# Optimization experiments

Measured on AMD Instinct MI355X. Metric: run time of the kernel, lower is better.

The kernel has to match this reference:

```python
import jax, jax.numpy as jnp
import numpy as np


def _gcn(x, edge_index, W, b):
    # PyG GCNConv, improved=True: A_hat = A + 2I, sym norm D^-1/2 A_hat D^-1/2
    N = x.shape[0]
    src, dst = edge_index[0], edge_index[1]
    h = x @ W  # [N, F]
    deg = jax.ops.segment_sum(jnp.ones(src.shape[0], x.dtype), dst, num_segments=N) + 2.0
    dinv = jax.lax.rsqrt(deg)
    norm = dinv[src] * dinv[dst]  # per-edge coefficient (edge_weight = 1)
    agg = jax.ops.segment_sum(h[src] * norm[:, None], dst, num_segments=N)
    agg = agg + (2.0 * dinv * dinv)[:, None] * h  # self loops, weight 2
    return agg + b


def _gclstm(x, H, C, Wx, Th, bch, wc, b):
    # GCLSTM with K=1: ChebConv on H reduces to H @ Theta + cheb_bias.
    # Gate order in stacked params: [i, f, c, o]; wc order: [i, f, o].
    gx = (jnp.einsum('nf,gfh->gnh', x, Wx)
          + jnp.einsum('nf,gfh->gnh', H, Th)
          + bch[:, None, :] + b[:, None, :])  # [4, N, F]
    I = jax.nn.sigmoid(gx[0] + wc[0] * C)
    Fg = jax.nn.sigmoid(gx[1] + wc[1] * C)
    Cn = Fg * C + I * jnp.tanh(gx[2])
    O = jax.nn.sigmoid(gx[3] + wc[2] * Cn)
    Hn = O * jnp.tanh(Cn)
    return Hn, Cn


def setup_inputs() -> dict:
    key = jax.random.key(0)
    ks = jax.random.split(key, 16)
    F = 2048
    E = 131072
    s = 0.02  # keep gates away from saturation
    inp = {
        'x': jax.random.normal(ks[0], (F, F), jnp.float32),
        'edge_index': jax.random.randint(ks[1], (2, E), 0, F),
        'no_pedestrians': F,
        'gcn1_w': s * jax.random.normal(ks[2], (F, F), jnp.float32),
        'gcn1_b': s * jax.random.normal(ks[3], (F,), jnp.float32),
        'gcn2_w': s * jax.random.normal(ks[4], (F, F), jnp.float32),
        'gcn2_b': s * jax.random.normal(ks[5], (F,), jnp.float32),
        'lstm_Wx': s * jax.random.normal(ks[6], (3, 4, F, F), jnp.float32),
        'lstm_Th': s * jax.random.normal(ks[7], (3, 4, F, F), jnp.float32),
        'lstm_bch': s * jax.random.normal(ks[8], (3, 4, F), jnp.float32),
        'lstm_wc': s * jax.random.normal(ks[9], (3, 3, F), jnp.float32),
        'lstm_b': s * jax.random.normal(ks[10], (3, 4, F), jnp.float32),
        'lin_w': s * jax.random.normal(ks[11], (9, F), jnp.float32),
        'lin_b': s * jax.random.normal(ks[12], (9,), jnp.float32),
    }
    return inp


def reference(x, edge_index, no_pedestrians, gcn1_w, gcn1_b, gcn2_w, gcn2_b,
              lstm_Wx, lstm_Th, lstm_bch, lstm_wc, lstm_b, lin_w, lin_b):
    # x is already [input_feat, input_feat], so the zero-padding in the
    # original forward is a no-op.
    h = jax.nn.relu(_gcn(x, edge_index, gcn1_w, gcn1_b))
    h = jax.nn.relu(_gcn(h, edge_index, gcn2_w, gcn2_b))
    N, F = h.shape
    z = jnp.zeros((N, F), h.dtype)
    H = h
    for l in range(3):  # 3 structurally distinct GCLSTM layers, single step
        H, _C = _gclstm(H, z, z, lstm_Wx[l], lstm_Th[l], lstm_bch[l], lstm_wc[l], lstm_b[l])
    h = jax.nn.relu(H)
    y = h @ lin_w.T + lin_b  # [N, 9]
    P = int(no_pedestrians)
    out = jax.nn.log_softmax(y[:P].reshape(P, 3, 3), axis=-1)  # LogSoftmax(dim=1) on each [3,3]
    return out
```

## Files before the change

### kernel.cpp

```cpp
#include <hip/hip_runtime.h>
#include <stdint.h>


#define FDIM 2048
typedef unsigned short u16;
typedef unsigned int u32;

typedef __bf16 bf16x8 __attribute__((ext_vector_type(8)));
typedef float f32x4 __attribute__((ext_vector_type(4)));
typedef __attribute__((address_space(1))) void* as1p;
typedef __attribute__((address_space(3))) void* as3p;

__device__ __forceinline__ float bflo(u32 u) { return __uint_as_float(u << 16); }
__device__ __forceinline__ float bfhi(u32 u) { return __uint_as_float(u & 0xffff0000u); }
__device__ __forceinline__ u16 f2b(float f) {
    u32 u = __float_as_uint(f);
    return (u16)((u + 0x7fffu + ((u >> 16) & 1u)) >> 16);
}
__device__ __forceinline__ void unp8(const uint4 v, float* f) {
    f[0] = bflo(v.x); f[1] = bfhi(v.x); f[2] = bflo(v.y); f[3] = bfhi(v.y);
    f[4] = bflo(v.z); f[5] = bfhi(v.z); f[6] = bflo(v.w); f[7] = bfhi(v.w);
}
__device__ __forceinline__ uint4 pk8(const float* f) {
    uint4 v;
    v.x = (u32)f2b(f[0]) | ((u32)f2b(f[1]) << 16);
    v.y = (u32)f2b(f[2]) | ((u32)f2b(f[3]) << 16);
    v.z = (u32)f2b(f[4]) | ((u32)f2b(f[5]) << 16);
    v.w = (u32)f2b(f[6]) | ((u32)f2b(f[7]) << 16);
    return v;
}

__global__ void k_zero(int* __restrict__ p, int n) {
    int i = blockIdx.x * 256 + threadIdx.x;
    if (i < n) p[i] = 0;
}

__global__ void k_hist(const int* __restrict__ ei, int* __restrict__ counts, int ne) {
    int e = blockIdx.x * 256 + threadIdx.x;
    if (e < ne) atomicAdd(&counts[ei[ne + e]], 1);
}

__global__ __launch_bounds__(1024) void k_scan(const int* __restrict__ counts,
                                               int* __restrict__ off,
                                               float* __restrict__ dinv) {
    __shared__ int sb[2][FDIM];
    const int t = threadIdx.x;
    const int c0 = counts[t], c1 = counts[t + 1024];
    sb[0][t] = c0; sb[0][t + 1024] = c1;
    __syncthreads();
    int cur = 0;
    for (int st = 1; st < FDIM; st <<= 1) {
        const int i1 = t + 1024;
        int v0 = sb[cur][t] + (t >= st ? sb[cur][t - st] : 0);
        int v1 = sb[cur][i1] + (i1 >= st ? sb[cur][i1 - st] : 0);
        sb[cur ^ 1][t] = v0; sb[cur ^ 1][i1] = v1;
        __syncthreads();
        cur ^= 1;
    }
    off[t] = sb[cur][t] - c0;
    off[t + 1024] = sb[cur][t + 1024] - c1;
    if (t == 0) off[FDIM] = sb[cur][FDIM - 1];
    dinv[t] = rsqrtf((float)c0 + 2.0f);
    dinv[t + 1024] = rsqrtf((float)c1 + 2.0f);
}

__global__ void k_fill(const int* __restrict__ ei, const int* __restrict__ off,
                       int* __restrict__ cursor, const float* __restrict__ dinv,
                       int* __restrict__ csr_s, float* __restrict__ csr_w, int ne) {
    int e = blockIdx.x * 256 + threadIdx.x;
    if (e >= ne) return;
    int s = ei[e], d = ei[ne + e];
    int p = atomicAdd(&cursor[d], 1);
    int idx = off[d] + p;
    csr_s[idx] = s;
    csr_w[idx] = dinv[s] * dinv[d];
}

__global__ void k_f2b8(const float* __restrict__ x, u16* __restrict__ o) {
    const int i = blockIdx.x * 256 + threadIdx.x;
    const size_t base = (size_t)i * 8;
    float f[8];
    *(float4*)(f)     = *(const float4*)(x + base);
    *(float4*)(f + 4) = *(const float4*)(x + base + 4);
    *(uint4*)(o + base) = pk8(f);
}

__global__ __launch_bounds__(1024) void k_transp(const float* __restrict__ W,
                                                 u16* __restrict__ Wt) {
    __shared__ float tile[32][33];
    const int tx = threadIdx.x & 31, ty = threadIdx.x >> 5;
    const int bx = blockIdx.x * 32, by = blockIdx.y * 32;
    tile[ty][tx] = W[(size_t)(by + ty) * FDIM + bx + tx];
    __syncthreads();
    Wt[(size_t)(bx + ty) * FDIM + by + tx] = f2b(tile[tx][ty]);
}

struct GemmArgs {
    const u16* A;
    const u16* Bt[3];
    u16* C[3];
    const float* b1[3];
    const float* b2[3];
};

__global__ __launch_bounds__(256) void k_gemm(GemmArgs ga) {
    const int z = blockIdx.z;
    const u16* __restrict__ A  = ga.A;
    const u16* __restrict__ Bt = ga.Bt[z];

    const int tid = threadIdx.x;
    const int wid = tid >> 6;
    const int lane = tid & 63;
    const int wr = wid >> 1, wc = wid & 1;
    const int lr = lane & 15, lg = lane >> 4;
    const int brow = blockIdx.y * 128;
    const int bcol = blockIdx.x * 128;

    __shared__ u16 As[128 * 32];
    __shared__ u16 Bs[128 * 32];

    f32x4 acc[4][4];
#pragma unroll
    for (int m = 0; m < 4; ++m)
#pragma unroll
        for (int n = 0; n < 4; ++n) acc[m][n] = (f32x4){0.f, 0.f, 0.f, 0.f};

    const u16* gA[2]; const u16* gB[2];
    u16* lA[2]; u16* lB[2];
#pragma unroll
    for (int q = 0; q < 2; ++q) {
        const int seg = q * 4 + wid;
        const int row = seg * 16 + (lane >> 2);
        const int ke  = (lane & 3) * 8;
        gA[q] = A  + (size_t)(brow + row) * FDIM + ke;
        gB[q] = Bt + (size_t)(bcol + row) * FDIM + ke;
        lA[q] = As + seg * 512;
        lB[q] = Bs + seg * 512;
    }

    int aoff[4], boff[4];
#pragma unroll
    for (int m = 0; m < 4; ++m) aoff[m] = (wr * 64 + m * 16 + lr) * 32 + lg * 8;
#pragma unroll
    for (int n = 0; n < 4; ++n) boff[n] = (wc * 64 + n * 16 + lr) * 32 + lg * 8;

    for (int kt = 0; kt < FDIM / 32; ++kt) {
        const int ko = kt * 32;
        __builtin_amdgcn_global_load_lds((as1p)(u16*)(gA[0] + ko), (as3p)lA[0], 16, 0, 0);
        __builtin_amdgcn_global_load_lds((as1p)(u16*)(gA[1] + ko), (as3p)lA[1], 16, 0, 0);
        __builtin_amdgcn_global_load_lds((as1p)(u16*)(gB[0] + ko), (as3p)lB[0], 16, 0, 0);
        __builtin_amdgcn_global_load_lds((as1p)(u16*)(gB[1] + ko), (as3p)lB[1], 16, 0, 0);
        __syncthreads();

        bf16x8 av[4], bv[4];
#pragma unroll
        for (int m = 0; m < 4; ++m) av[m] = *reinterpret_cast<const bf16x8*>(&As[aoff[m]]);
#pragma unroll
        for (int n = 0; n < 4; ++n) bv[n] = *reinterpret_cast<const bf16x8*>(&Bs[boff[n]]);
#pragma unroll
        for (int m = 0; m < 4; ++m)
#pragma unroll
            for (int n = 0; n < 4; ++n)
                acc[m][n] = __builtin_amdgcn_mfma_f32_16x16x32_bf16(av[m], bv[n], acc[m][n], 0, 0, 0);
        __syncthreads();
    }

    u16* __restrict__ C = ga.C[z];
    const float* b1 = ga.b1[z];
    const float* b2 = ga.b2[z];
#pragma unroll
    for (int n = 0; n < 4; ++n) {
        const int col = bcol + wc * 64 + n * 16 + lr;
        float badd = 0.f;
        if (b1) badd = b1[col] + b2[col];
#pragma unroll
        for (int m = 0; m < 4; ++m) {
            const int row0 = brow + wr * 64 + m * 16 + lg * 4;
#pragma unroll
            for (int r = 0; r < 4; ++r)
                C[(size_t)(row0 + r) * FDIM + col] = f2b(acc[m][n][r] + badd);
        }
    }
}

__global__ __launch_bounds__(256) void k_gather(
    const u16* __restrict__ Hp, const int* __restrict__ off,
    const int* __restrict__ csr_s, const float* __restrict__ csr_w,
    const float* __restrict__ dinv, const float* __restrict__ bias,
    u16* __restrict__ outb) {
    const int n = blockIdx.x, t = threadIdx.x;
    __shared__ int s_src[256];
    __shared__ float s_w[256];
    float acc[8] = {0.f, 0.f, 0.f, 0.f, 0.f, 0.f, 0.f, 0.f};
    const int e0 = off[n], e1 = off[n + 1];
    const int fb = t * 8;
    for (int base = e0; base < e1; base += 256) {
        const int cnt = min(256, e1 - base);
        __syncthreads();
        if (t < cnt) { s_src[t] = csr_s[base + t]; s_w[t] = csr_w[base + t]; }
        __syncthreads();
        for (int i = 0; i < cnt; ++i) {
            const int s = s_src[i];
            const float w = s_w[i];
            const uint4 v = *reinterpret_cast<const uint4*>(Hp + (size_t)s * FDIM + fb);
            float f[8]; unp8(v, f);
#pragma unroll
            for (int j = 0; j < 8; ++j) acc[j] = fmaf(w, f[j], acc[j]);
        }
    }
    const float di = dinv[n];
    const float sw = 2.f * di * di;
    {
        const uint4 v = *reinterpret_cast<const uint4*>(Hp + (size_t)n * FDIM + fb);
        float f[8]; unp8(v, f);
#pragma unroll
        for (int j = 0; j < 8; ++j) acc[j] = fmaf(sw, f[j], acc[j]);
    }
    float bb[8];
    *(float4*)(bb)     = *(const float4*)(bias + fb);
    *(float4*)(bb + 4) = *(const float4*)(bias + fb + 4);
    float r[8];
#pragma unroll
    for (int j = 0; j < 8; ++j) r[j] = fmaxf(acc[j] + bb[j], 0.f);
    *reinterpret_cast<uint4*>(outb + (size_t)n * FDIM + fb) = pk8(r);
}

__global__ void k_lstm_act(const u16* gi, const u16* __restrict__ gc,
                           const u16* __restrict__ go, const float* __restrict__ wc2,
                           u16* Ho) {
    const int i = blockIdx.x * 256 + threadIdx.x;
    const size_t base = (size_t)i * 8;
    const int f = (int)(base & (FDIM - 1));
    const uint4 vi = *(const uint4*)(gi + base);
    const uint4 vc = *(const uint4*)(gc + base);
    const uint4 vo = *(const uint4*)(go + base);
    float fi[8], fc[8], fo[8], w[8], h[8];
    unp8(vi, fi); unp8(vc, fc); unp8(vo, fo);
    *(float4*)(w)     = *(const float4*)(wc2 + f);
    *(float4*)(w + 4) = *(const float4*)(wc2 + f + 4);
#pragma unroll
    for (int j = 0; j < 8; ++j) {
        const float I  = 1.f / (1.f + __expf(-fi[j]));
        const float Cn = I * tanhf(fc[j]);
        const float O  = 1.f / (1.f + __expf(-(fo[j] + w[j] * Cn)));
        h[j] = O * tanhf(Cn);
    }
    *(uint4*)(Ho + base) = pk8(h);
}

__global__ __launch_bounds__(256) void k_final(const u16* __restrict__ Hf,
                                               const float* __restrict__ lw,
                                               const float* __restrict__ lb,
                                               float* __restrict__ out) {
    const int n = blockIdx.x, t = threadIdx.x;
    float p[9] = {0.f, 0.f, 0.f, 0.f, 0.f, 0.f, 0.f, 0.f, 0.f};
    for (int f = t; f < FDIM; f += 256) {
        float h = __uint_as_float(((u32)Hf[(size_t)n * FDIM + f]) << 16);
        h = fmaxf(h, 0.f);
#pragma unroll
        for (int j = 0; j < 9; ++j) p[j] = fmaf(h, lw[j * FDIM + f], p[j]);
    }
    __shared__ float red[9][256];
#pragma unroll
    for (int j = 0; j < 9; ++j) red[j][t] = p[j];
    __syncthreads();
    for (int s = 128; s > 0; s >>= 1) {
        if (t < s) {
#pragma unroll
            for (int j = 0; j < 9; ++j) red[j][t] += red[j][t + s];
        }
        __syncthreads();
    }
    if (t == 0) {
        float y[9];
#pragma unroll
        for (int j = 0; j < 9; ++j) y[j] = red[j][0] + lb[j];
#pragma unroll
        for (int g = 0; g < 3; ++g) {
            const float a = y[g * 3], b = y[g * 3 + 1], c = y[g * 3 + 2];
            const float m = fmaxf(a, fmaxf(b, c));
            const float lse = m + logf(__expf(a - m) + __expf(b - m) + __expf(c - m));
            out[n * 9 + g * 3 + 0] = a - lse;
            out[n * 9 + g * 3 + 1] = b - lse;
            out[n * 9 + g * 3 + 2] = c - lse;
        }
    }
}

extern "C" void kernel_launch(void* const* d_in, const int* in_sizes, int n_in,
                              void* d_out, int out_size, void* d_ws, size_t ws_size,
                              hipStream_t stream) {
    const float* x   = (const float*)d_in[0];
    const int*   ei  = (const int*)d_in[1];
    const float* g1w = (const float*)d_in[3];
    const float* g1b = (const float*)d_in[4];
    const float* g2w = (const float*)d_in[5];
    const float* g2b = (const float*)d_in[6];
    const float* Wx  = (const float*)d_in[7];
    const float* bch = (const float*)d_in[9];
    const float* wcv = (const float*)d_in[10];
    const float* bb  = (const float*)d_in[11];
    const float* lw  = (const float*)d_in[12];
    const float* lb  = (const float*)d_in[13];
    float* out = (float*)d_out;

    const int NE = in_sizes[1] / 2;
    const size_t FF = (size_t)FDIM * FDIM;

    const size_t BUF = (FF * 2 + 255) & ~(size_t)255;
    const size_t csr_bytes = ((size_t)FDIM * 8 + ((size_t)FDIM + 1) * 4 + (size_t)FDIM * 4
                              + (size_t)NE * 8 + 4 * 256);
    const size_t needed = 7 * BUF + csr_bytes;

    char* wp = (char*)d_ws;
    bool fallback = (ws_size < needed);
    auto alloc = [&](size_t bytes) -> void* {
        if (fallback) return d_ws;
        void* p = (void*)wp;
        wp += (bytes + 255) & ~(size_t)255;
        return p;
    };
    u16* A0 = (u16*)alloc(FF * 2);
    u16* A1 = (u16*)alloc(FF * 2);
    u16* G1 = (u16*)alloc(FF * 2);
    u16* G2 = (u16*)alloc(FF * 2);
    u16* WT0 = (u16*)alloc(FF * 2);
    u16* WT1 = (u16*)alloc(FF * 2);
    u16* WT2 = (u16*)alloc(FF * 2);
    int*   counts;
    int*   off;
    float* dinv;
    int*   csr_s;
    float* csr_w;
    if (!fallback) {
        counts = (int*)alloc((size_t)FDIM * 4 * 2);
        off    = (int*)alloc(((size_t)FDIM + 1) * 4);
        dinv   = (float*)alloc((size_t)FDIM * 4);
        csr_s  = (int*)alloc((size_t)NE * 4);
        csr_w  = (float*)alloc((size_t)NE * 4);
    } else {
        char* base = (char*)d_ws;
        counts = (int*)base;
        off    = (int*)(base + (size_t)64 * 1024);
        dinv   = (float*)(base + (size_t)128 * 1024);
        csr_s  = (int*)(base + (size_t)1024 * 1024);
        csr_w  = (float*)(base + (size_t)2048 * 1024);
    }
    int* cursor = counts + FDIM;

    const int eb = (NE + 255) / 256;
    const dim3 tg(64, 64), tb(1024);
    const dim3 gb(256);

    k_zero<<<dim3((2 * FDIM + 255) / 256), dim3(256), 0, stream>>>(counts, 2 * FDIM);
    k_hist<<<dim3(eb), dim3(256), 0, stream>>>(ei, counts, NE);
    k_scan<<<dim3(1), dim3(1024), 0, stream>>>(counts, off, dinv);
    k_fill<<<dim3(eb), dim3(256), 0, stream>>>(ei, off, cursor, dinv, csr_s, csr_w, NE);

    k_f2b8<<<dim3(2048), dim3(256), 0, stream>>>(x, A0);

    GemmArgs ga;
    k_transp<<<tg, tb, 0, stream>>>(g1w, WT0);
    ga.A = A0;
    for (int s = 0; s < 3; ++s) { ga.Bt[s] = WT0; ga.C[s] = A1; ga.b1[s] = nullptr; ga.b2[s] = nullptr; }
    k_gemm<<<dim3(16, 16, 1), gb, 0, stream>>>(ga);
    k_gather<<<dim3(FDIM), dim3(256), 0, stream>>>(A1, off, csr_s, csr_w, dinv, g1b, G1);
    k_transp<<<tg, tb, 0, stream>>>(g2w, WT0);
    ga.A = G1;
    k_gemm<<<dim3(16, 16, 1), gb, 0, stream>>>(ga);
    k_gather<<<dim3(FDIM), dim3(256), 0, stream>>>(A1, off, csr_s, csr_w, dinv, g2b, A0);

    u16* cur = A0;
    u16* alt = A1;
    for (int l = 0; l < 3; ++l) {
        const int gsel[3] = {0, 2, 3};
        u16* wts[3]   = {WT0, WT1, WT2};
        u16* gouts[3] = {alt, G1, G2};
        for (int s = 0; s < 3; ++s)
            k_transp<<<tg, tb, 0, stream>>>(Wx + (size_t)(l * 4 + gsel[s]) * FF, wts[s]);
        GemmArgs gl;
        gl.A = cur;
        for (int s = 0; s < 3; ++s) {
            gl.Bt[s] = wts[s];
            gl.C[s]  = gouts[s];
            gl.b1[s] = bch + (size_t)(l * 4 + gsel[s]) * FDIM;
            gl.b2[s] = bb  + (size_t)(l * 4 + gsel[s]) * FDIM;
        }
        k_gemm<<<dim3(16, 16, 3), gb, 0, stream>>>(gl);
        k_lstm_act<<<dim3(2048), dim3(256), 0, stream>>>(alt, G1, G2,
                                                         wcv + (size_t)(l * 3 + 2) * FDIM, alt);
        u16* tmp = cur; cur = alt; alt = tmp;
    }

    k_final<<<dim3(FDIM), dim3(256), 0, stream>>>(cur, lw, lb, out);
}
```

Before: 871.4 us.

## Batch all weight transposes into one launch and split-K the GCN GEMMs

All eleven weight transposes now run in a single 3D-grid launch at the start instead of eleven separate launches spread through the pipeline, with one workspace buffer holding every transposed weight. The two single-output GCN GEMMs, which only fill 256 blocks, are split along K into two halves that write fp32 partial sums, and a new combine kernel adds the halves and converts them to bf16. This is meant to cut launch overhead and raise GPU occupancy for the small GEMMs. The cost is about 32 MB of extra fp32 partial traffic per GCN layer, an extra kernel per layer, and a much larger workspace requirement that may trigger the aliased fallback path.

```diff
diff --git a/kernel.cpp b/kernel.cpp
--- a/kernel.cpp
+++ b/kernel.cpp
@@ -85,8 +85,10 @@
     *(uint4*)(o + base) = pk8(f);
 }
 
-__global__ __launch_bounds__(1024) void k_transp(const float* __restrict__ W,
-                                                 u16* __restrict__ Wt) {
+struct TranspArgs { const float* W[11]; u16* WT; };
+__global__ __launch_bounds__(1024) void k_transp_all(TranspArgs ta) {
+    const float* __restrict__ W = ta.W[blockIdx.z];
+    u16* __restrict__ Wt = ta.WT + (size_t)blockIdx.z * FDIM * FDIM;
     __shared__ float tile[32][33];
     const int tx = threadIdx.x & 31, ty = threadIdx.x >> 5;
     const int bx = blockIdx.x * 32, by = blockIdx.y * 32;
@@ -181,6 +183,95 @@
                 C[(size_t)(row0 + r) * FDIM + col] = f2b(acc[m][n][r] + badd);
         }
     }
+}
+
+__global__ __launch_bounds__(256) void k_gemm_sk(const u16* __restrict__ A,
+                                                const u16* __restrict__ Bt,
+                                                float* __restrict__ P) {
+    const int kz = blockIdx.z;
+    const int tid = threadIdx.x;
+    const int wid = tid >> 6;
+    const int lane = tid & 63;
+    const int wr = wid >> 1, wc = wid & 1;
+    const int lr = lane & 15, lg = lane >> 4;
+    const int brow = blockIdx.y * 128;
+    const int bcol = blockIdx.x * 128;
+
+    __shared__ u16 As[128 * 32];
+    __shared__ u16 Bs[128 * 32];
+
+    f32x4 acc[4][4];
+#pragma unroll
+    for (int m = 0; m < 4; ++m)
+#pragma unroll
+        for (int n = 0; n < 4; ++n) acc[m][n] = (f32x4){0.f, 0.f, 0.f, 0.f};
+
+    const u16* gA[2]; const u16* gB[2];
+    u16* lA[2]; u16* lB[2];
+#pragma unroll
+    for (int q = 0; q < 2; ++q) {
+        const int seg = q * 4 + wid;
+        const int row = seg * 16 + (lane >> 2);
+        const int ke  = (lane & 3) * 8;
+        gA[q] = A  + (size_t)(brow + row) * FDIM + kz * 1024 + ke;
+        gB[q] = Bt + (size_t)(bcol + row) * FDIM + kz * 1024 + ke;
+        lA[q] = As + seg * 512;
+        lB[q] = Bs + seg * 512;
+    }
+
+    int aoff[4], boff[4];
+#pragma unroll
+    for (int m = 0; m < 4; ++m) aoff[m] = (wr * 64 + m * 16 + lr) * 32 + lg * 8;
+#pragma unroll
+    for (int n = 0; n < 4; ++n) boff[n] = (wc * 64 + n * 16 + lr) * 32 + lg * 8;
+
+    for (int kt = 0; kt < 1024 / 32; ++kt) {
+        const int ko = kt * 32;
+        __builtin_amdgcn_global_load_lds((as1p)(u16*)(gA[0] + ko), (as3p)lA[0], 16, 0, 0);
+        __builtin_amdgcn_global_load_lds((as1p)(u16*)(gA[1] + ko), (as3p)lA[1], 16, 0, 0);
+        __builtin_amdgcn_global_load_lds((as1p)(u16*)(gB[0] + ko), (as3p)lB[0], 16, 0, 0);
+        __builtin_amdgcn_global_load_lds((as1p)(u16*)(gB[1] + ko), (as3p)lB[1], 16, 0, 0);
+        __syncthreads();
+
+        bf16x8 av[4], bv[4];
+#pragma unroll
+        for (int m = 0; m < 4; ++m) av[m] = *reinterpret_cast<const bf16x8*>(&As[aoff[m]]);
+#pragma unroll
+        for (int n = 0; n < 4; ++n) bv[n] = *reinterpret_cast<const bf16x8*>(&Bs[boff[n]]);
+#pragma unroll
+        for (int m = 0; m < 4; ++m)
+#pragma unroll
+            for (int n = 0; n < 4; ++n)
+                acc[m][n] = __builtin_amdgcn_mfma_f32_16x16x32_bf16(av[m], bv[n], acc[m][n], 0, 0, 0);
+        __syncthreads();
+    }
+
+    float* __restrict__ Pz = P + (size_t)kz * FDIM * FDIM;
+#pragma unroll
+    for (int n = 0; n < 4; ++n) {
+        const int col = bcol + wc * 64 + n * 16 + lr;
+#pragma unroll
+        for (int m = 0; m < 4; ++m) {
+            const int row0 = brow + wr * 64 + m * 16 + lg * 4;
+#pragma unroll
+            for (int r = 0; r < 4; ++r)
+                Pz[(size_t)(row0 + r) * FDIM + col] = acc[m][n][r];
+        }
+    }
+}
+
+__global__ void k_comb(const float* __restrict__ P, u16* __restrict__ o) {
+    const int i = blockIdx.x * 256 + threadIdx.x;
+    const size_t base = (size_t)i * 8;
+    const size_t FF = (size_t)FDIM * FDIM;
+    float a[8], b[8], f[8];
+    *(float4*)(a)     = *(const float4*)(P + base);
+    *(float4*)(a + 4) = *(const float4*)(P + base + 4);
+    *(float4*)(b)     = *(const float4*)(P + FF + base);
+    *(float4*)(b + 4) = *(const float4*)(P + FF + base + 4);
+#pragma unroll
+    for (int j = 0; j < 8; ++j) f[j] = a[j] + b[j];
+    *(uint4*)(o + base) = pk8(f);
 }
 
 __global__ __launch_bounds__(256) void k_gather(
@@ -306,11 +397,12 @@
 
     const int NE = in_sizes[1] / 2;
     const size_t FF = (size_t)FDIM * FDIM;
+    const int gsel[3] = {0, 2, 3};
 
     const size_t BUF = (FF * 2 + 255) & ~(size_t)255;
     const size_t csr_bytes = ((size_t)FDIM * 8 + ((size_t)FDIM + 1) * 4 + (size_t)FDIM * 4
                               + (size_t)NE * 8 + 4 * 256);
-    const size_t needed = 7 * BUF + csr_bytes;
+    const size_t needed = 4 * BUF + 11 * BUF + 2 * FF * 4 + csr_bytes + 1024;
 
     char* wp = (char*)d_ws;
     bool fallback = (ws_size < needed);
@@ -320,13 +412,12 @@
         wp += (bytes + 255) & ~(size_t)255;
         return p;
     };
-    u16* A0 = (u16*)alloc(FF * 2);
-    u16* A1 = (u16*)alloc(FF * 2);
-    u16* G1 = (u16*)alloc(FF * 2);
-    u16* G2 = (u16*)alloc(FF * 2);
-    u16* WT0 = (u16*)alloc(FF * 2);
-    u16* WT1 = (u16*)alloc(FF * 2);
-    u16* WT2 = (u16*)alloc(FF * 2);
+    u16* A0  = (u16*)alloc(FF * 2);
+    u16* A1  = (u16*)alloc(FF * 2);
+    u16* G1  = (u16*)alloc(FF * 2);
+    u16* G2  = (u16*)alloc(FF * 2);
+    u16* WT  = (u16*)alloc(11 * FF * 2);
+    float* Pf = (float*)alloc(2 * FF * 4);
     int*   counts;
     int*   off;
     float* dinv;
@@ -349,8 +440,16 @@
     int* cursor = counts + FDIM;
 
     const int eb = (NE + 255) / 256;
-    const dim3 tg(64, 64), tb(1024);
     const dim3 gb(256);
+
+    TranspArgs ta;
+    ta.W[0] = g1w;
+    ta.W[1] = g2w;
+    for (int l = 0; l < 3; ++l)
+        for (int s = 0; s < 3; ++s)
+            ta.W[2 + l * 3 + s] = Wx + (size_t)(l * 4 + gsel[s]) * FF;
+    ta.WT = WT;
+    k_transp_all<<<dim3(64, 64, 11), dim3(1024), 0, stream>>>(ta);
 
     k_zero<<<dim3((2 * FDIM + 255) / 256), dim3(256), 0, stream>>>(counts, 2 * FDIM);
     k_hist<<<dim3(eb), dim3(256), 0, stream>>>(ei, counts, NE);
@@ -359,29 +458,21 @@
 
     k_f2b8<<<dim3(2048), dim3(256), 0, stream>>>(x, A0);
 
-    GemmArgs ga;
-    k_transp<<<tg, tb, 0, stream>>>(g1w, WT0);
-    ga.A = A0;
-    for (int s = 0; s < 3; ++s) { ga.Bt[s] = WT0; ga.C[s] = A1; ga.b1[s] = nullptr; ga.b2[s] = nullptr; }
-    k_gemm<<<dim3(16, 16, 1), gb, 0, stream>>>(ga);
+    k_gemm_sk<<<dim3(16, 16, 2), gb, 0, stream>>>(A0, WT, Pf);
+    k_comb<<<dim3(2048), dim3(256), 0, stream>>>(Pf, A1);
     k_gather<<<dim3(FDIM), dim3(256), 0, stream>>>(A1, off, csr_s, csr_w, dinv, g1b, G1);
-    k_transp<<<tg, tb, 0, stream>>>(g2w, WT0);
-    ga.A = G1;
-    k_gemm<<<dim3(16, 16, 1), gb, 0, stream>>>(ga);
+    k_gemm_sk<<<dim3(16, 16, 2), gb, 0, stream>>>(G1, WT + FF, Pf);
+    k_comb<<<dim3(2048), dim3(256), 0, stream>>>(Pf, A1);
     k_gather<<<dim3(FDIM), dim3(256), 0, stream>>>(A1, off, csr_s, csr_w, dinv, g2b, A0);
 
     u16* cur = A0;
     u16* alt = A1;
     for (int l = 0; l < 3; ++l) {
-        const int gsel[3] = {0, 2, 3};
-        u16* wts[3]   = {WT0, WT1, WT2};
         u16* gouts[3] = {alt, G1, G2};
-        for (int s = 0; s < 3; ++s)
-            k_transp<<<tg, tb, 0, stream>>>(Wx + (size_t)(l * 4 + gsel[s]) * FF, wts[s]);
         GemmArgs gl;
         gl.A = cur;
         for (int s = 0; s < 3; ++s) {
-            gl.Bt[s] = wts[s];
+            gl.Bt[s] = WT + (size_t)(2 + l * 3 + s) * FF;
             gl.C[s]  = gouts[s];
             gl.b1[s] = bch + (size_t)(l * 4 + gsel[s]) * FDIM;
             gl.b2[s] = bb  + (size_t)(l * 4 + gsel[s]) * FDIM;
```

After: 870.1 us. No clear change (-0.1%).
